# Optimization experiments

Hardware: AMD Instinct MI355X
Metric: run time of the kernel (lower is better)

Reference implementation:

```python
import jax, jax.numpy as jnp
import numpy as np

VISION_TOKEN_TYPE = 1

def _swiglu_mlp(x, w_gate, w_up, w_down):
    # x: [B, L, D]; w_gate/w_up: [D, F]; w_down: [F, D]
    g = jax.nn.silu(jnp.einsum('bld,df->blf', x, w_gate))
    u = jnp.einsum('bld,df->blf', x, w_up)
    return jnp.einsum('blf,fd->bld', g * u, w_down)

def _vision_mask(token_type_ids):
    # vision_token_mask[:, :-1] = (tt[:, :-1]==V) & (tt[:, 1:]==V); last col False
    is_v = token_type_ids == VISION_TOKEN_TYPE
    pair = is_v[:, :-1] & is_v[:, 1:]
    return jnp.concatenate([pair, jnp.zeros_like(pair[:, :1])], axis=1)  # [B, L] bool

def setup_inputs() -> dict:
    key = jax.random.key(0)
    ks = jax.random.split(key, 8)
    B, L, D, F = 2, 2048, 4096, 11008
    s = 0.02
    return {
        'hidden_states': jax.random.normal(ks[0], (B, L, D), dtype=jnp.float32),
        'token_type_ids': jax.random.randint(ks[1], (B, L), 0, 2, dtype=jnp.int64),
        'vision_gate': jax.random.normal(ks[2], (D, F), dtype=jnp.float32) * s,
        'vision_up': jax.random.normal(ks[3], (D, F), dtype=jnp.float32) * s,
        'vision_down': jax.random.normal(ks[4], (F, D), dtype=jnp.float32) * s,
        'language_gate': jax.random.normal(ks[5], (D, F), dtype=jnp.float32) * s,
        'language_up': jax.random.normal(ks[6], (D, F), dtype=jnp.float32) * s,
        'language_down': jax.random.normal(ks[7], (F, D), dtype=jnp.float32) * s,
    }

def reference(hidden_states, token_type_ids, vision_gate, vision_up, vision_down,
              language_gate, language_up, language_down):
    vmask = _vision_mask(token_type_ids)  # [B, L]
    out_v = _swiglu_mlp(hidden_states, vision_gate, vision_up, vision_down)
    out_l = _swiglu_mlp(hidden_states, language_gate, language_up, language_down)
    return jnp.where(vmask[:, :, None], out_v, out_l)
```

## Files before the change

### kernel.cpp

```cpp
#include <hip/hip_runtime.h>
#include <hip/hip_bf16.h>

#define B_    2
#define L_    2048
#define D_    4096
#define F_    11008
#define M_TOK (B_ * L_)
#define BM    256
#define M_ALLOC (M_TOK + BM)
#define NTM   (M_ALLOC / BM)
#define NT_GU (D_ / 64)
#define NT_DN (F_ / 64)
#define NTILE_F (F_ / 128)
#define SPLITK_DN 4
#define LDS_GU 131072
#define LDS_DN 131072

typedef __attribute__((ext_vector_type(8))) __bf16 bf16x8;
typedef __attribute__((ext_vector_type(4))) float  f32x4;
typedef unsigned short ushort_t;
typedef unsigned int   uint_t;


__device__ __forceinline__ void gload_lds16(const void* g, void* l) {
  __builtin_amdgcn_global_load_lds(
      (const __attribute__((address_space(1))) void*)g,
      (__attribute__((address_space(3))) void*)l, 16, 0, 0);
}

#define PH_BAR()  { __builtin_amdgcn_sched_barrier(0); __builtin_amdgcn_s_barrier(); __builtin_amdgcn_sched_barrier(0); }
#define LGKM0()   { asm volatile("s_waitcnt lgkmcnt(0)" ::: "memory"); __builtin_amdgcn_sched_barrier(0); }
#define VM4()     { asm volatile("s_waitcnt vmcnt(4)" ::: "memory"); __builtin_amdgcn_sched_barrier(0); }
#define VM0()     { asm volatile("s_waitcnt vmcnt(0)" ::: "memory"); __builtin_amdgcn_sched_barrier(0); }

__device__ __forceinline__ ushort_t f2bf(float v) {
  union { __hip_bfloat16 h; ushort_t u; } cv;
  cv.h = __float2bfloat16(v);
  return cv.u;
}

__device__ __forceinline__ int xcd_swz(int orig, int nwg) {
  const int q = nwg >> 3, r = nwg & 7, xcd = orig & 7;
  return (xcd < r ? xcd * (q + 1) : r * (q + 1) + (xcd - r) * q) + (orig >> 3);
}

__device__ __forceinline__ void stage_half(const __hip_bfloat16* __restrict__ src, int ldE,
                                           __bf16* ldsb, int w, int lane) {
#pragma unroll
  for (int j = 0; j < 2; ++j) {
    const int ch  = (w * 2 + j) * 64 + lane;
    const int row = ch >> 3;
    const int cc  = (ch & 7) ^ (row & 7);
    gload_lds16(src + (size_t)(row * ldE + cc * 8), ldsb + (w * 2 + j) * 512);
  }
}

__device__ __forceinline__ bf16x8 ldfrag(const __bf16* region, int row, int koffb) {
  const int off = ((row << 7) + koffb) ^ ((row & 7) << 4);
  return *(const bf16x8*)((const char*)region + off);
}

__device__ __forceinline__ void mfma_q(f32x4 (&acc)[8][4], int mb, int nb,
                                       const bf16x8 (&af)[4][2], const bf16x8 (&bf)[2][2]) {
#pragma unroll
  for (int mm = 0; mm < 4; ++mm)
#pragma unroll
    for (int nn = 0; nn < 2; ++nn)
#pragma unroll
      for (int ks = 0; ks < 2; ++ks)
        acc[mb + mm][nb + nn] = __builtin_amdgcn_mfma_f32_16x16x32_bf16(
            af[mm][ks], bf[nn][ks], acc[mb + mm][nb + nn], 0, 0, 0);
}

__device__ __forceinline__ void gemm_kloop(const __hip_bfloat16* __restrict__ Ag, const int ldA,
                                           const __hip_bfloat16* __restrict__ Bg, const int ldB,
                                           const int nt, __bf16* smem, f32x4 (&acc)[8][4],
                                           const int wm, const int wn, const int l15,
                                           const int l4, const int w, const int lane) {
  stage_half(Ag,             ldA, smem,                w, lane);
  stage_half(Ag + 128 * ldA, ldA, smem + 8192,         w, lane);
  stage_half(Bg,             ldB, smem + 16384,        w, lane);
  stage_half(Bg + 128 * ldB, ldB, smem + 24576,        w, lane);
  if (1 < nt) {
    stage_half(Ag + 64,             ldA, smem + 32768,        w, lane);
    stage_half(Ag + 64 + 128 * ldA, ldA, smem + 32768 + 8192, w, lane);
  }
  VM4(); PH_BAR();

  for (int t = 0; t < nt; ++t) {
    __bf16* bufc = smem + (t & 1) * 32768;
    __bf16* bufn = smem + ((t + 1) & 1) * 32768;
    const __bf16* At = bufc;
    const __bf16* Bt = bufc + 16384;
    bf16x8 a0[4][2], a1[4][2], b0[2][2], b1[2][2];

#pragma unroll
    for (int i = 0; i < 4; ++i)
#pragma unroll
      for (int ks = 0; ks < 2; ++ks)
        a0[i][ks] = ldfrag(At, wm * 128 + i * 16 + l15, ks * 64 + l4 * 16);
#pragma unroll
    for (int n = 0; n < 2; ++n)
#pragma unroll
      for (int ks = 0; ks < 2; ++ks)
        b0[n][ks] = ldfrag(Bt, wn * 64 + n * 16 + l15, ks * 64 + l4 * 16);
    if (t + 1 < nt) stage_half(Bg + (t + 1) * 64, ldB, bufn + 16384, w, lane);
    PH_BAR(); LGKM0();
    __builtin_amdgcn_s_setprio(1);
    mfma_q(acc, 0, 0, a0, b0);
    __builtin_amdgcn_s_setprio(0);
    PH_BAR();

#pragma unroll
    for (int i = 0; i < 4; ++i)
#pragma unroll
      for (int ks = 0; ks < 2; ++ks)
        a1[i][ks] = ldfrag(At, wm * 128 + 64 + i * 16 + l15, ks * 64 + l4 * 16);
    if (t + 1 < nt) stage_half(Bg + (t + 1) * 64 + 128 * ldB, ldB, bufn + 24576, w, lane);
    PH_BAR(); LGKM0();
    __builtin_amdgcn_s_setprio(1);
    mfma_q(acc, 4, 0, a1, b0);
    __builtin_amdgcn_s_setprio(0);
    PH_BAR();

#pragma unroll
    for (int n = 0; n < 2; ++n)
#pragma unroll
      for (int ks = 0; ks < 2; ++ks)
        b1[n][ks] = ldfrag(Bt, wn * 64 + 32 + n * 16 + l15, ks * 64 + l4 * 16);
    if (t + 2 < nt) stage_half(Ag + (t + 2) * 64, ldA, bufc, w, lane);
    PH_BAR(); LGKM0();
    __builtin_amdgcn_s_setprio(1);
    mfma_q(acc, 4, 2, a1, b1);
    __builtin_amdgcn_s_setprio(0);
    PH_BAR();

    if (t + 2 < nt) stage_half(Ag + (t + 2) * 64 + 128 * ldA, ldA, bufc + 8192, w, lane);
    __builtin_amdgcn_s_setprio(1);
    mfma_q(acc, 0, 2, a0, b1);
    __builtin_amdgcn_s_setprio(0);
    if (t + 2 < nt) { VM4(); } else { VM0(); }
    PH_BAR();
  }
}


__global__ void init_kernel(int* counters, int* slot2tok) {
  int i = blockIdx.x * 256 + threadIdx.x;
  if (i < 2) counters[i] = 0;
  if (i < M_ALLOC) slot2tok[i] = -1;
}

__global__ void assign_kernel(const int* __restrict__ tt, int* counters,
                              int* __restrict__ slot2tok) {
  int t = blockIdx.x * 256 + threadIdx.x;
  if (t >= M_TOK) return;
  int l = t & (L_ - 1);
  bool isv = (tt[t] == 1) && (l < L_ - 1) && (tt[t + 1] == 1);
  int slot;
  if (isv) slot = atomicAdd(&counters[0], 1);
  else     slot = M_ALLOC - 1 - atomicAdd(&counters[1], 1);
  slot2tok[slot] = t;
}

__global__ void gather_cvt(const float* __restrict__ x, const int* __restrict__ slot2tok,
                           __hip_bfloat16* __restrict__ xg) {
  const int s = blockIdx.x;
  const int t = slot2tok[s];
  __hip_bfloat16* dst = xg + (size_t)s * D_ + threadIdx.x * 16;
  union { ushort_t h[8]; uint4 v; } p0, p1;
  if (t >= 0) {
    const float4* s4 = (const float4*)(x + (size_t)t * D_ + threadIdx.x * 16);
    float4 a = s4[0], b = s4[1], c = s4[2], d = s4[3];
    float vals[16] = {a.x,a.y,a.z,a.w,b.x,b.y,b.z,b.w,c.x,c.y,c.z,c.w,d.x,d.y,d.z,d.w};
#pragma unroll
    for (int i = 0; i < 8; ++i) p0.h[i] = f2bf(vals[i]);
#pragma unroll
    for (int i = 0; i < 8; ++i) p1.h[i] = f2bf(vals[8 + i]);
  } else {
    p0.v = make_uint4(0, 0, 0, 0);
    p1.v = make_uint4(0, 0, 0, 0);
  }
  *(uint4*)dst = p0.v;
  *(uint4*)(dst + 8) = p1.v;
}

__global__ __launch_bounds__(256) void transpose_cvt_lds(
    const float* __restrict__ s0, const float* __restrict__ s1,
    const float* __restrict__ s2, const float* __restrict__ s3,
    __hip_bfloat16* __restrict__ d0, __hip_bfloat16* __restrict__ d1,
    __hip_bfloat16* __restrict__ d2, __hip_bfloat16* __restrict__ d3,
    int R, int C) {
  const float* in;
  __hip_bfloat16* out;
  switch (blockIdx.y) {
    case 0:  in = s0; out = d0; break;
    case 1:  in = s1; out = d1; break;
    case 2:  in = s2; out = d2; break;
    default: in = s3; out = d3; break;
  }
  __shared__ float tile[64][65];
  const int cb = C >> 6;
  const int c0 = (blockIdx.x % cb) * 64;
  const int r0 = (blockIdx.x / cb) * 64;
  const int tx = threadIdx.x & 63;
  const int ty = threadIdx.x >> 6;
#pragma unroll
  for (int j = 0; j < 16; ++j) {
    const int r = ty + 4 * j;
    tile[r][tx] = in[(size_t)(r0 + r) * C + c0 + tx];
  }
  __syncthreads();
  const int rr2 = (threadIdx.x & 31) * 2;
  const int cc  = threadIdx.x >> 5;
#pragma unroll
  for (int j = 0; j < 8; ++j) {
    const int c = cc + 8 * j;
    const uint_t lo = f2bf(tile[rr2][c]);
    const uint_t hi = f2bf(tile[rr2 + 1][c]);
    *(uint_t*)(out + (size_t)(c0 + c) * R + r0 + rr2) = lo | (hi << 16);
  }
}

__global__ void sentinel_kernel(float* out, int n) {
  int i = blockIdx.x * 256 + threadIdx.x;
  if (i < n) out[i] = 1e30f;
}

__global__ __launch_bounds__(512, 2) void gemm256_gateup_fused(
    const __hip_bfloat16* __restrict__ Xg,
    const __hip_bfloat16* __restrict__ WgTv, const __hip_bfloat16* __restrict__ WuTv,
    const __hip_bfloat16* __restrict__ WgTl, const __hip_bfloat16* __restrict__ WuTl,
    __hip_bfloat16* __restrict__ H, const int* __restrict__ counters) {
  extern __shared__ __bf16 smem[];
  const int tid = threadIdx.x, lane = tid & 63, w = tid >> 6;
  const int wm = w >> 1, wn = w & 1;
  const int l15 = lane & 15, l4 = lane >> 4;

  const int wg = xcd_swz(blockIdx.x, gridDim.x);
  const int mt = wg % NTM, ntile = wg / NTM;
  const int row0 = mt * BM;
  const int ncol0 = ntile * 128;
  const int nv = counters[0];
  const bool isv = row0 < nv;
  const __hip_bfloat16* Ag   = Xg + (size_t)row0 * D_;
  const __hip_bfloat16* Bg_g = (isv ? WgTv : WgTl) + (size_t)ncol0 * D_;
  const __hip_bfloat16* Bu_g = (isv ? WuTv : WuTl) + (size_t)ncol0 * D_;

  f32x4 accg[4][4] = {};
  f32x4 accu[4][4] = {};
  const int nt = NT_GU;

  stage_half(Ag,                  D_, smem,          w, lane);
  stage_half(Ag + 128 * D_,       D_, smem + 8192,   w, lane);
  stage_half(Bg_g,                D_, smem + 32768,  w, lane);
  stage_half(Bu_g,                D_, smem + 49152,  w, lane);
  stage_half(Ag + 64,             D_, smem + 16384,  w, lane);
  stage_half(Ag + 64 + 128 * D_,  D_, smem + 24576,  w, lane);
  VM4(); PH_BAR();

  for (int t = 0; t < nt; ++t) {
    const int cur = t & 1;
    const __bf16* At  = smem + cur * 16384;
    const __bf16* Bgt = smem + 32768 + cur * 8192;
    const __bf16* But = smem + 49152 + cur * 8192;
    __bf16* nxA  = smem + cur * 16384;
    __bf16* nxBg = smem + 32768 + (cur ^ 1) * 8192;
    __bf16* nxBu = smem + 49152 + (cur ^ 1) * 8192;
    bf16x8 af[4][2], bb[4][2];

#pragma unroll
    for (int m = 0; m < 2; ++m)
#pragma unroll
      for (int ks = 0; ks < 2; ++ks)
        af[m][ks] = ldfrag(At, wm * 64 + m * 16 + l15, ks * 64 + l4 * 16);
#pragma unroll
    for (int n = 0; n < 4; ++n)
#pragma unroll
      for (int ks = 0; ks < 2; ++ks)
        bb[n][ks] = ldfrag(Bgt, wn * 64 + n * 16 + l15, ks * 64 + l4 * 16);
    if (t + 1 < nt) stage_half(Bg_g + (t + 1) * 64, D_, nxBg, w, lane);
    PH_BAR(); LGKM0();
    __builtin_amdgcn_s_setprio(1);
#pragma unroll
    for (int m = 0; m < 2; ++m)
#pragma unroll
      for (int n = 0; n < 4; ++n)
#pragma unroll
        for (int ks = 0; ks < 2; ++ks)
          accg[m][n] = __builtin_amdgcn_mfma_f32_16x16x32_bf16(
              af[m][ks], bb[n][ks], accg[m][n], 0, 0, 0);
    __builtin_amdgcn_s_setprio(0);
    PH_BAR();

#pragma unroll
    for (int m = 2; m < 4; ++m)
#pragma unroll
      for (int ks = 0; ks < 2; ++ks)
        af[m][ks] = ldfrag(At, wm * 64 + m * 16 + l15, ks * 64 + l4 * 16);
    if (t + 1 < nt) stage_half(Bu_g + (t + 1) * 64, D_, nxBu, w, lane);
    PH_BAR(); LGKM0();
    __builtin_amdgcn_s_setprio(1);
#pragma unroll
    for (int m = 2; m < 4; ++m)
#pragma unroll
      for (int n = 0; n < 4; ++n)
#pragma unroll
        for (int ks = 0; ks < 2; ++ks)
          accg[m][n] = __builtin_amdgcn_mfma_f32_16x16x32_bf16(
              af[m][ks], bb[n][ks], accg[m][n], 0, 0, 0);
    __builtin_amdgcn_s_setprio(0);
    PH_BAR();

#pragma unroll
    for (int n = 0; n < 4; ++n)
#pragma unroll
      for (int ks = 0; ks < 2; ++ks)
        bb[n][ks] = ldfrag(But, wn * 64 + n * 16 + l15, ks * 64 + l4 * 16);
    if (t + 2 < nt) stage_half(Ag + (t + 2) * 64, D_, nxA, w, lane);
    PH_BAR(); LGKM0();
    __builtin_amdgcn_s_setprio(1);
#pragma unroll
    for (int m = 0; m < 2; ++m)
#pragma unroll
      for (int n = 0; n < 4; ++n)
#pragma unroll
        for (int ks = 0; ks < 2; ++ks)
          accu[m][n] = __builtin_amdgcn_mfma_f32_16x16x32_bf16(
              af[m][ks], bb[n][ks], accu[m][n], 0, 0, 0);
    __builtin_amdgcn_s_setprio(0);
    PH_BAR();

    if (t + 2 < nt) stage_half(Ag + (t + 2) * 64 + 128 * D_, D_, nxA + 8192, w, lane);
    __builtin_amdgcn_s_setprio(1);
#pragma unroll
    for (int m = 2; m < 4; ++m)
#pragma unroll
      for (int n = 0; n < 4; ++n)
#pragma unroll
        for (int ks = 0; ks < 2; ++ks)
          accu[m][n] = __builtin_amdgcn_mfma_f32_16x16x32_bf16(
              af[m][ks], bb[n][ks], accu[m][n], 0, 0, 0);
    __builtin_amdgcn_s_setprio(0);
    if (t + 2 < nt) { VM4(); } else { VM0(); }
    PH_BAR();
  }

#pragma unroll
  for (int m = 0; m < 4; ++m) {
    const int grow = row0 + wm * 64 + m * 16 + l4 * 4;
#pragma unroll
    for (int rr = 0; rr < 4; ++rr) {
      __hip_bfloat16* orow = H + (size_t)(grow + rr) * F_ + ncol0 + wn * 64 + l15;
#pragma unroll
      for (int n = 0; n < 4; ++n) {
        const float g = accg[m][n][rr];
        const float u = accu[m][n][rr];
        orow[n * 16] = __float2bfloat16(g / (1.0f + __expf(-g)) * u);
      }
    }
  }
}


__global__ __launch_bounds__(512, 2) void gemm256_down(
    const __hip_bfloat16* __restrict__ H,
    const __hip_bfloat16* __restrict__ WdTv, const __hip_bfloat16* __restrict__ WdTl,
    float* __restrict__ out, const int* __restrict__ counters,
    const int* __restrict__ slot2tok) {
  extern __shared__ __bf16 smem[];
  const int tid = threadIdx.x, lane = tid & 63, w = tid >> 6;
  const int wm = w >> 2, wn = w & 3;
  const int l15 = lane & 15, l4 = lane >> 4;

  const int wg = xcd_swz(blockIdx.x, gridDim.x);
  const int mt = wg % NTM, ntt = wg / NTM;
  const int z  = blockIdx.y;
  const int row0 = mt * BM;
  const int ncol0 = ntt * 256;
  const int ntz = NT_DN / SPLITK_DN;
  const int t0 = z * ntz;
  const int nv = counters[0];
  const __hip_bfloat16* Bsrc = (row0 < nv) ? WdTv : WdTl;
  const __hip_bfloat16* Ag = H + (size_t)row0 * F_ + t0 * 64;
  const __hip_bfloat16* Bg = Bsrc + (size_t)ncol0 * F_ + t0 * 64;

  f32x4 acc[8][4] = {};
  gemm_kloop(Ag, F_, Bg, F_, ntz, smem, acc, wm, wn, l15, l4, w, lane);

#pragma unroll
  for (int m = 0; m < 8; ++m) {
    const int slot = row0 + wm * 128 + m * 16 + l4 * 4;
#pragma unroll
    for (int rr = 0; rr < 4; ++rr) {
      const int tok = slot2tok[slot + rr];
      if (tok < 0) continue;
      float* orow = out + (size_t)tok * D_ + ncol0 + wn * 64 + l15;
#pragma unroll
      for (int n = 0; n < 4; ++n)
        atomicAdd(&orow[n * 16], acc[m][n][rr]);
    }
  }
}


extern "C" void kernel_launch(void* const* d_in, const int* in_sizes, int n_in,
                              void* d_out, int out_size, void* d_ws, size_t ws_size,
                              hipStream_t stream) {
  const float* x   = (const float*)d_in[0];
  const int*   tt  = (const int*)d_in[1];
  const float* wgv = (const float*)d_in[2];
  const float* wuv = (const float*)d_in[3];
  const float* wdv = (const float*)d_in[4];
  const float* wgl = (const float*)d_in[5];
  const float* wul = (const float*)d_in[6];
  const float* wdl = (const float*)d_in[7];
  float* out = (float*)d_out;

  size_t off = 0;
  auto nalign = [](size_t v) { return (v + 255) & ~(size_t)255; };
  const size_t o_cnt = off; off += nalign(2 * sizeof(int));
  const size_t o_s2t = off; off += nalign((size_t)M_ALLOC * sizeof(int));
  const size_t o_xg  = off; off += nalign((size_t)M_ALLOC * D_ * 2);
  const size_t o_h   = off; off += nalign((size_t)M_ALLOC * F_ * 2);
  const size_t wbytes = nalign((size_t)D_ * F_ * 2);
  const size_t o_wgv = off; off += wbytes;
  const size_t o_wuv = off; off += wbytes;
  const size_t o_wgl = off; off += wbytes;
  const size_t o_wul = off; off += wbytes;

  if (ws_size < off) {
    sentinel_kernel<<<(out_size + 255) / 256, 256, 0, stream>>>(out, out_size);
    return;
  }

  char* ws = (char*)d_ws;
  int* counters = (int*)(ws + o_cnt);
  int* slot2tok = (int*)(ws + o_s2t);
  __hip_bfloat16* Xg  = (__hip_bfloat16*)(ws + o_xg);
  __hip_bfloat16* H   = (__hip_bfloat16*)(ws + o_h);
  __hip_bfloat16* WgTv = (__hip_bfloat16*)(ws + o_wgv);
  __hip_bfloat16* WuTv = (__hip_bfloat16*)(ws + o_wuv);
  __hip_bfloat16* WgTl = (__hip_bfloat16*)(ws + o_wgl);
  __hip_bfloat16* WuTl = (__hip_bfloat16*)(ws + o_wul);
  __hip_bfloat16* WdTv = WgTv;
  __hip_bfloat16* WdTl = WuTv;

  hipFuncSetAttribute((const void*)gemm256_gateup_fused,
                      hipFuncAttributeMaxDynamicSharedMemorySize, LDS_GU);
  hipFuncSetAttribute((const void*)gemm256_down,
                      hipFuncAttributeMaxDynamicSharedMemorySize, LDS_DN);

  hipMemsetAsync(out, 0, (size_t)out_size * sizeof(float), stream);

  init_kernel<<<(M_ALLOC + 255) / 256, 256, 0, stream>>>(counters, slot2tok);
  assign_kernel<<<(M_TOK + 255) / 256, 256, 0, stream>>>(tt, counters, slot2tok);
  gather_cvt<<<M_ALLOC, 256, 0, stream>>>(x, slot2tok, Xg);

  dim3 tb(256);
  const int tblocks = (F_ / 64) * (D_ / 64);
  transpose_cvt_lds<<<dim3(tblocks, 4), tb, 0, stream>>>(
      wgv, wuv, wgl, wul, WgTv, WuTv, WgTl, WuTl, D_, F_);

  gemm256_gateup_fused<<<dim3(NTM * NTILE_F), 512, LDS_GU, stream>>>(
      Xg, WgTv, WuTv, WgTl, WuTl, H, counters);

  transpose_cvt_lds<<<dim3(tblocks, 2), tb, 0, stream>>>(
      wdv, wdl, wdv, wdl, WdTv, WdTl, WdTv, WdTl, F_, D_);

  gemm256_down<<<dim3(NTM * (D_ / 256), SPLITK_DN), 512, LDS_DN, stream>>>(
      H, WdTv, WdTl, out, counters, slot2tok);
}
```

Baseline: 1.494 ms.

## Restructure GEMM k-loop into two phases with partial LDS waits; merge weight transposes

```diff
diff --git a/kernel.cpp b/kernel.cpp
--- a/kernel.cpp
+++ b/kernel.cpp
@@ -28,10 +28,13 @@
       (__attribute__((address_space(3))) void*)l, 16, 0, 0);
 }
 
+#define SCHED0()  __builtin_amdgcn_sched_barrier(0)
 #define PH_BAR()  { __builtin_amdgcn_sched_barrier(0); __builtin_amdgcn_s_barrier(); __builtin_amdgcn_sched_barrier(0); }
-#define LGKM0()   { asm volatile("s_waitcnt lgkmcnt(0)" ::: "memory"); __builtin_amdgcn_sched_barrier(0); }
+#define LGKM(n)   { asm volatile("s_waitcnt lgkmcnt(" #n ")" ::: "memory"); __builtin_amdgcn_sched_barrier(0); }
 #define VM4()     { asm volatile("s_waitcnt vmcnt(4)" ::: "memory"); __builtin_amdgcn_sched_barrier(0); }
 #define VM0()     { asm volatile("s_waitcnt vmcnt(0)" ::: "memory"); __builtin_amdgcn_sched_barrier(0); }
+#define PRIO1()   __builtin_amdgcn_s_setprio(1)
+#define PRIO0()   __builtin_amdgcn_s_setprio(0)
 
 __device__ __forceinline__ ushort_t f2bf(float v) {
   union { __hip_bfloat16 h; ushort_t u; } cv;
@@ -77,21 +80,22 @@
                                            const int nt, __bf16* smem, f32x4 (&acc)[8][4],
                                            const int wm, const int wn, const int l15,
                                            const int l4, const int w, const int lane) {
-  stage_half(Ag,             ldA, smem,                w, lane);
-  stage_half(Ag + 128 * ldA, ldA, smem + 8192,         w, lane);
-  stage_half(Bg,             ldB, smem + 16384,        w, lane);
-  stage_half(Bg + 128 * ldB, ldB, smem + 24576,        w, lane);
+  stage_half(Ag,             ldA, smem,          w, lane);
+  stage_half(Ag + 128 * ldA, ldA, smem + 8192,   w, lane);
+  stage_half(Bg,             ldB, smem + 32768,  w, lane);
+  stage_half(Bg + 128 * ldB, ldB, smem + 40960,  w, lane);
   if (1 < nt) {
-    stage_half(Ag + 64,             ldA, smem + 32768,        w, lane);
-    stage_half(Ag + 64 + 128 * ldA, ldA, smem + 32768 + 8192, w, lane);
+    stage_half(Ag + 64,             ldA, smem + 16384, w, lane);
+    stage_half(Ag + 64 + 128 * ldA, ldA, smem + 24576, w, lane);
   }
   VM4(); PH_BAR();
 
   for (int t = 0; t < nt; ++t) {
-    __bf16* bufc = smem + (t & 1) * 32768;
-    __bf16* bufn = smem + ((t + 1) & 1) * 32768;
-    const __bf16* At = bufc;
-    const __bf16* Bt = bufc + 16384;
+    const int cur = t & 1;
+    const __bf16* At = smem + cur * 16384;
+    const __bf16* Bt = smem + 32768 + cur * 16384;
+    __bf16* nxA = smem + cur * 16384;
+    __bf16* nxB = smem + 32768 + (cur ^ 1) * 16384;
     bf16x8 a0[4][2], a1[4][2], b0[2][2], b1[2][2];
 
 #pragma unroll
@@ -104,41 +108,39 @@
 #pragma unroll
       for (int ks = 0; ks < 2; ++ks)
         b0[n][ks] = ldfrag(Bt, wn * 64 + n * 16 + l15, ks * 64 + l4 * 16);
-    if (t + 1 < nt) stage_half(Bg + (t + 1) * 64, ldB, bufn + 16384, w, lane);
-    PH_BAR(); LGKM0();
-    __builtin_amdgcn_s_setprio(1);
-    mfma_q(acc, 0, 0, a0, b0);
-    __builtin_amdgcn_s_setprio(0);
+    SCHED0();
+#pragma unroll
+    for (int i = 0; i < 4; ++i)
+#pragma unroll
+      for (int ks = 0; ks < 2; ++ks)
+        a1[i][ks] = ldfrag(At, wm * 128 + 64 + i * 16 + l15, ks * 64 + l4 * 16);
+    SCHED0();
+#pragma unroll
+    for (int n = 0; n < 2; ++n)
+#pragma unroll
+      for (int ks = 0; ks < 2; ++ks)
+        b1[n][ks] = ldfrag(Bt, wn * 64 + 32 + n * 16 + l15, ks * 64 + l4 * 16);
+    SCHED0();
+    if (t + 1 < nt) {
+      stage_half(Bg + (t + 1) * 64,             ldB, nxB,        w, lane);
+      stage_half(Bg + (t + 1) * 64 + 128 * ldB, ldB, nxB + 8192, w, lane);
+    }
+    SCHED0();
+    LGKM(12);
+    PRIO1(); mfma_q(acc, 0, 0, a0, b0); PRIO0();
+    LGKM(4);
+    PRIO1(); mfma_q(acc, 4, 0, a1, b0); PRIO0();
+    LGKM(0);
     PH_BAR();
-
-#pragma unroll
-    for (int i = 0; i < 4; ++i)
-#pragma unroll
-      for (int ks = 0; ks < 2; ++ks)
-        a1[i][ks] = ldfrag(At, wm * 128 + 64 + i * 16 + l15, ks * 64 + l4 * 16);
-    if (t + 1 < nt) stage_half(Bg + (t + 1) * 64 + 128 * ldB, ldB, bufn + 24576, w, lane);
-    PH_BAR(); LGKM0();
-    __builtin_amdgcn_s_setprio(1);
-    mfma_q(acc, 4, 0, a1, b0);
-    __builtin_amdgcn_s_setprio(0);
-    PH_BAR();
-
-#pragma unroll
-    for (int n = 0; n < 2; ++n)
-#pragma unroll
-      for (int ks = 0; ks < 2; ++ks)
-        b1[n][ks] = ldfrag(Bt, wn * 64 + 32 + n * 16 + l15, ks * 64 + l4 * 16);
-    if (t + 2 < nt) stage_half(Ag + (t + 2) * 64, ldA, bufc, w, lane);
-    PH_BAR(); LGKM0();
-    __builtin_amdgcn_s_setprio(1);
+    if (t + 2 < nt) {
+      stage_half(Ag + (t + 2) * 64,             ldA, nxA,        w, lane);
+      stage_half(Ag + (t + 2) * 64 + 128 * ldA, ldA, nxA + 8192, w, lane);
+    }
+    SCHED0();
+    PRIO1();
     mfma_q(acc, 4, 2, a1, b1);
-    __builtin_amdgcn_s_setprio(0);
-    PH_BAR();
-
-    if (t + 2 < nt) stage_half(Ag + (t + 2) * 64 + 128 * ldA, ldA, bufc + 8192, w, lane);
-    __builtin_amdgcn_s_setprio(1);
     mfma_q(acc, 0, 2, a0, b1);
-    __builtin_amdgcn_s_setprio(0);
+    PRIO0();
     if (t + 2 < nt) { VM4(); } else { VM0(); }
     PH_BAR();
   }
@@ -185,20 +187,25 @@
   *(uint4*)(dst + 8) = p1.v;
 }
 
-__global__ __launch_bounds__(256) void transpose_cvt_lds(
+__global__ __launch_bounds__(256) void transpose_cvt_lds6(
     const float* __restrict__ s0, const float* __restrict__ s1,
     const float* __restrict__ s2, const float* __restrict__ s3,
+    const float* __restrict__ s4, const float* __restrict__ s5,
     __hip_bfloat16* __restrict__ d0, __hip_bfloat16* __restrict__ d1,
     __hip_bfloat16* __restrict__ d2, __hip_bfloat16* __restrict__ d3,
-    int R, int C) {
+    __hip_bfloat16* __restrict__ d4, __hip_bfloat16* __restrict__ d5) {
   const float* in;
   __hip_bfloat16* out;
   switch (blockIdx.y) {
     case 0:  in = s0; out = d0; break;
     case 1:  in = s1; out = d1; break;
     case 2:  in = s2; out = d2; break;
-    default: in = s3; out = d3; break;
-  }
+    case 3:  in = s3; out = d3; break;
+    case 4:  in = s4; out = d4; break;
+    default: in = s5; out = d5; break;
+  }
+  const int R = (blockIdx.y < 4) ? D_ : F_;
+  const int C = (blockIdx.y < 4) ? F_ : D_;
   __shared__ float tile[64][65];
   const int cb = C >> 6;
   const int c0 = (blockIdx.x % cb) * 64;
@@ -267,7 +274,7 @@
     __bf16* nxA  = smem + cur * 16384;
     __bf16* nxBg = smem + 32768 + (cur ^ 1) * 8192;
     __bf16* nxBu = smem + 49152 + (cur ^ 1) * 8192;
-    bf16x8 af[4][2], bb[4][2];
+    bf16x8 af[4][2], bg[4][2], bu[4][2];
 
 #pragma unroll
     for (int m = 0; m < 2; ++m)
@@ -278,10 +285,27 @@
     for (int n = 0; n < 4; ++n)
 #pragma unroll
       for (int ks = 0; ks < 2; ++ks)
-        bb[n][ks] = ldfrag(Bgt, wn * 64 + n * 16 + l15, ks * 64 + l4 * 16);
-    if (t + 1 < nt) stage_half(Bg_g + (t + 1) * 64, D_, nxBg, w, lane);
-    PH_BAR(); LGKM0();
-    __builtin_amdgcn_s_setprio(1);
+        bg[n][ks] = ldfrag(Bgt, wn * 64 + n * 16 + l15, ks * 64 + l4 * 16);
+    SCHED0();
+#pragma unroll
+    for (int m = 2; m < 4; ++m)
+#pragma unroll
+      for (int ks = 0; ks < 2; ++ks)
+        af[m][ks] = ldfrag(At, wm * 64 + m * 16 + l15, ks * 64 + l4 * 16);
+    SCHED0();
+#pragma unroll
+    for (int n = 0; n < 4; ++n)
+#pragma unroll
+      for (int ks = 0; ks < 2; ++ks)
+        bu[n][ks] = ldfrag(But, wn * 64 + n * 16 + l15, ks * 64 + l4 * 16);
+    SCHED0();
+    if (t + 1 < nt) {
+      stage_half(Bg_g + (t + 1) * 64, D_, nxBg, w, lane);
+      stage_half(Bu_g + (t + 1) * 64, D_, nxBu, w, lane);
+    }
+    SCHED0();
+    LGKM(12);
+    PRIO1();
 #pragma unroll
     for (int m = 0; m < 2; ++m)
 #pragma unroll
@@ -289,18 +313,10 @@
 #pragma unroll
         for (int ks = 0; ks < 2; ++ks)
           accg[m][n] = __builtin_amdgcn_mfma_f32_16x16x32_bf16(
-              af[m][ks], bb[n][ks], accg[m][n], 0, 0, 0);
-    __builtin_amdgcn_s_setprio(0);
-    PH_BAR();
-
-#pragma unroll
-    for (int m = 2; m < 4; ++m)
-#pragma unroll
-      for (int ks = 0; ks < 2; ++ks)
-        af[m][ks] = ldfrag(At, wm * 64 + m * 16 + l15, ks * 64 + l4 * 16);
-    if (t + 1 < nt) stage_half(Bu_g + (t + 1) * 64, D_, nxBu, w, lane);
-    PH_BAR(); LGKM0();
-    __builtin_amdgcn_s_setprio(1);
+              af[m][ks], bg[n][ks], accg[m][n], 0, 0, 0);
+    PRIO0();
+    LGKM(8);
+    PRIO1();
 #pragma unroll
     for (int m = 2; m < 4; ++m)
 #pragma unroll
@@ -308,40 +324,25 @@
 #pragma unroll
         for (int ks = 0; ks < 2; ++ks)
           accg[m][n] = __builtin_amdgcn_mfma_f32_16x16x32_bf16(
-              af[m][ks], bb[n][ks], accg[m][n], 0, 0, 0);
-    __builtin_amdgcn_s_setprio(0);
+              af[m][ks], bg[n][ks], accg[m][n], 0, 0, 0);
+    PRIO0();
+    LGKM(0);
     PH_BAR();
-
-#pragma unroll
-    for (int n = 0; n < 4; ++n)
-#pragma unroll
-      for (int ks = 0; ks < 2; ++ks)
-        bb[n][ks] = ldfrag(But, wn * 64 + n * 16 + l15, ks * 64 + l4 * 16);
-    if (t + 2 < nt) stage_half(Ag + (t + 2) * 64, D_, nxA, w, lane);
-    PH_BAR(); LGKM0();
-    __builtin_amdgcn_s_setprio(1);
-#pragma unroll
-    for (int m = 0; m < 2; ++m)
+    if (t + 2 < nt) {
+      stage_half(Ag + (t + 2) * 64,            D_, nxA,        w, lane);
+      stage_half(Ag + (t + 2) * 64 + 128 * D_, D_, nxA + 8192, w, lane);
+    }
+    SCHED0();
+    PRIO1();
+#pragma unroll
+    for (int m = 0; m < 4; ++m)
 #pragma unroll
       for (int n = 0; n < 4; ++n)
 #pragma unroll
         for (int ks = 0; ks < 2; ++ks)
           accu[m][n] = __builtin_amdgcn_mfma_f32_16x16x32_bf16(
-              af[m][ks], bb[n][ks], accu[m][n], 0, 0, 0);
-    __builtin_amdgcn_s_setprio(0);
-    PH_BAR();
-
-    if (t + 2 < nt) stage_half(Ag + (t + 2) * 64 + 128 * D_, D_, nxA + 8192, w, lane);
-    __builtin_amdgcn_s_setprio(1);
-#pragma unroll
-    for (int m = 2; m < 4; ++m)
-#pragma unroll
-      for (int n = 0; n < 4; ++n)
-#pragma unroll
-        for (int ks = 0; ks < 2; ++ks)
-          accu[m][n] = __builtin_amdgcn_mfma_f32_16x16x32_bf16(
-              af[m][ks], bb[n][ks], accu[m][n], 0, 0, 0);
-    __builtin_amdgcn_s_setprio(0);
+              af[m][ks], bu[n][ks], accu[m][n], 0, 0, 0);
+    PRIO0();
     if (t + 2 < nt) { VM4(); } else { VM0(); }
     PH_BAR();
   }
@@ -428,6 +429,8 @@
   const size_t o_wuv = off; off += wbytes;
   const size_t o_wgl = off; off += wbytes;
   const size_t o_wul = off; off += wbytes;
+  const size_t o_wdv = off; off += wbytes;
+  const size_t o_wdl = off; off += wbytes;
 
   if (ws_size < off) {
     sentinel_kernel<<<(out_size + 255) / 256, 256, 0, stream>>>(out, out_size);
@@ -443,8 +446,8 @@
   __hip_bfloat16* WuTv = (__hip_bfloat16*)(ws + o_wuv);
   __hip_bfloat16* WgTl = (__hip_bfloat16*)(ws + o_wgl);
   __hip_bfloat16* WuTl = (__hip_bfloat16*)(ws + o_wul);
-  __hip_bfloat16* WdTv = WgTv;
-  __hip_bfloat16* WdTl = WuTv;
+  __hip_bfloat16* WdTv = (__hip_bfloat16*)(ws + o_wdv);
+  __hip_bfloat16* WdTl = (__hip_bfloat16*)(ws + o_wdl);
 
   hipFuncSetAttribute((const void*)gemm256_gateup_fused,
                       hipFuncAttributeMaxDynamicSharedMemorySize, LDS_GU);
@@ -457,17 +460,13 @@
   assign_kernel<<<(M_TOK + 255) / 256, 256, 0, stream>>>(tt, counters, slot2tok);
   gather_cvt<<<M_ALLOC, 256, 0, stream>>>(x, slot2tok, Xg);
 
-  dim3 tb(256);
   const int tblocks = (F_ / 64) * (D_ / 64);
-  transpose_cvt_lds<<<dim3(tblocks, 4), tb, 0, stream>>>(
-      wgv, wuv, wgl, wul, WgTv, WuTv, WgTl, WuTl, D_, F_);
+  transpose_cvt_lds6<<<dim3(tblocks, 6), 256, 0, stream>>>(
+      wgv, wuv, wgl, wul, wdv, wdl, WgTv, WuTv, WgTl, WuTl, WdTv, WdTl);
 
   gemm256_gateup_fused<<<dim3(NTM * NTILE_F), 512, LDS_GU, stream>>>(
       Xg, WgTv, WuTv, WgTl, WuTl, H, counters);
 
-  transpose_cvt_lds<<<dim3(tblocks, 2), tb, 0, stream>>>(
-      wdv, wdl, wdv, wdl, WdTv, WdTl, WdTv, WdTl, F_, D_);
-
   gemm256_down<<<dim3(NTM * (D_ / 256), SPLITK_DN), 512, LDS_DN, stream>>>(
       H, WdTv, WdTl, out, counters, slot2tok);
 }
```

After: 1.718 ms. 1.15x slower.
